# Performance work log

Hardware: AMD Instinct MI355X
Metric: run time of the kernel (lower is better)

## Reference

```python
import jax, jax.numpy as jnp
import numpy as np

N = 50000
E = 800000
EL = 100000
IN_CH = 33
HID = 64
OUT = 128
NTYPES = 311
EMB = 16
COMB = IN_CH - 1 + EMB  # 48


def setup_inputs() -> dict:
    key = jax.random.key(0)
    ks = jax.random.split(key, 24)
    # x: col 0 = node type (integer-valued float), rest = float features
    types = jax.random.randint(ks[0], (N, 1), 0, NTYPES).astype(jnp.float32)
    feats = jax.random.normal(ks[1], (N, IN_CH - 1), dtype=jnp.float32)
    x = jnp.concatenate([types, feats], axis=1)
    edge_index = jax.random.randint(ks[2], (2, E), 0, N, dtype=jnp.int32)
    edge_label_index = jax.random.randint(ks[3], (2, EL), 0, N, dtype=jnp.int32)
    s = 0.05
    inp = {
        'x': x, 'edge_index': edge_index, 'edge_label_index': edge_label_index,
        'emb': jax.random.normal(ks[4], (NTYPES, EMB)) * s,
        'W1': jax.random.normal(ks[5], (COMB, 4 * HID)) * s,
        'a_src1': jax.random.normal(ks[6], (4, HID)) * s,
        'a_dst1': jax.random.normal(ks[7], (4, HID)) * s,
        'b1': jnp.zeros((4 * HID,)),
        'W2': jax.random.normal(ks[8], (4 * HID, 2 * 2 * HID)) * s,
        'a_src2': jax.random.normal(ks[9], (2, 2 * HID)) * s,
        'a_dst2': jax.random.normal(ks[10], (2, 2 * HID)) * s,
        'b2': jnp.zeros((2 * 2 * HID,)),
        'W3': jax.random.normal(ks[11], (4 * HID, OUT)) * s,
        'a_src3': jax.random.normal(ks[12], (1, OUT)) * s,
        'a_dst3': jax.random.normal(ks[13], (1, OUT)) * s,
        'b3': jnp.zeros((OUT,)),
        'Wl1': jax.random.normal(ks[14], (2 * OUT, HID)) * s,
        'bl1': jnp.zeros((HID,)),
        'Wl2': jax.random.normal(ks[15], (HID, 1)) * s,
        'bl2': jnp.zeros((1,)),
        'trans_bias': jax.random.normal(ks[16], (NTYPES, NTYPES)) * s,
    }
    return inp


def _gat(h_in, src, dst, W, a_src, a_dst, b, heads, d_out):
    # linear transform, per-head split
    h = (h_in @ W).reshape(N, heads, d_out)                      # [N,H,D]
    al_s = jnp.einsum('nhd,hd->nh', h, a_src)                    # [N,H]
    al_d = jnp.einsum('nhd,hd->nh', h, a_dst)
    logits = jax.nn.leaky_relu(al_s[src] + al_d[dst], 0.2)       # [E,H]
    m = jax.ops.segment_max(logits, dst, num_segments=N)
    m = jnp.where(jnp.isfinite(m), m, 0.0)
    e = jnp.exp(logits - m[dst])
    denom = jax.ops.segment_sum(e, dst, num_segments=N)
    alpha = e / (denom[dst] + 1e-16)                             # [E,H]
    msg = h[src] * alpha[:, :, None]                             # [E,H,D]
    out = jax.ops.segment_sum(msg, dst, num_segments=N)          # [N,H,D]
    return out.reshape(N, heads * d_out) + b


def reference(x, edge_index, edge_label_index, emb, W1, a_src1, a_dst1, b1,
              W2, a_src2, a_dst2, b2, W3, a_src3, a_dst3, b3,
              Wl1, bl1, Wl2, bl2, trans_bias):
    node_types = x[:, 0].astype(jnp.int32)
    x_comb = jnp.concatenate([emb[node_types], x[:, 1:]], axis=1)  # [N,48]
    # add self loops (PyG GATConv default)
    loops = jnp.arange(N, dtype=edge_index.dtype)
    ei = jnp.concatenate([edge_index, jnp.stack([loops, loops])], axis=1)
    src, dst = ei[0], ei[1]
    z = jax.nn.elu(_gat(x_comb, src, dst, W1, a_src1, a_dst1, b1, 4, HID))
    z = jax.nn.elu(_gat(z, src, dst, W2, a_src2, a_dst2, b2, 2, 2 * HID))
    z = _gat(z, src, dst, W3, a_src3, a_dst3, b3, 1, OUT)
    # decode
    ls, ld = edge_label_index[0], edge_label_index[1]
    ef = jnp.concatenate([z[ls], z[ld]], axis=1)                  # [EL,2*OUT]
    h = jax.nn.relu(ef @ Wl1 + bl1)
    base = h @ Wl2 + bl2                                          # [EL,1]
    bias = trans_bias[node_types[ls], node_types[ld]][:, None]
    return base + bias
```

## Files before the change

kernel.cpp:

```cpp
#include <hip/hip_runtime.h>
#include <hip/hip_bf16.h>

#define NN 50000
#define EE 800000
#define ELN 100000
#define ETOT (EE + NN)
#define NT 311

#define NBUCK ((NN + 127) >> 7)
#define BCAP 3072
#define CHUNK 8192

#define SB_CVT 512
#define SB_PRE (SB_CVT)
#define SB_BC  (SB_CVT + 1)
#define SB_ZS  (SB_CVT + 2)
#define ZS_N   (NN * 6)
#define SB_TOT (SB_ZS + (ZS_N + 255) / 256)

typedef _Float16 f16;
typedef f16 f16x8 __attribute__((ext_vector_type(8)));
typedef f16 f16x4 __attribute__((ext_vector_type(4)));
typedef f16 f16x2 __attribute__((ext_vector_type(2)));
typedef float f32x4 __attribute__((ext_vector_type(4)));

__device__ __forceinline__ float edge_alpha(float l)
{
    l = l > 0.f ? l : 0.2f * l;
    return __expf(fminf(l, 80.f));
}

__global__ __launch_bounds__(256) void k_prepatt(const float* __restrict__ x,
                                                 const float* __restrict__ emb,
                                                 const float* __restrict__ a1ps,
                                                 const float* __restrict__ a1pd,
                                                 f16* __restrict__ xc,
                                                 int* __restrict__ ntypes,
                                                 float* __restrict__ als,
                                                 float* __restrict__ ald)
{
    int gid = blockIdx.x * 256 + threadIdx.x;
    int n = gid >> 6, lane = gid & 63;
    if (n >= NN) return;
    int tpe = (int)x[(size_t)n * 33];
    tpe = tpe < 0 ? 0 : (tpe > NT - 1 ? NT - 1 : tpe);
    if (lane == 0) ntypes[n] = tpe;
    float v;
    if (lane < 16)      v = emb[tpe * 16 + lane];
    else if (lane < 48) v = x[(size_t)n * 33 + 1 + (lane - 16)];
    else                v = 0.f;
    f16 hv = (f16)v;
    xc[(size_t)n * 64 + lane] = hv;
    float xv = (float)hv;
    float ps[4], pd[4];
    #pragma unroll
    for (int h = 0; h < 4; ++h) {
        ps[h] = xv * a1ps[h * 64 + lane];
        pd[h] = xv * a1pd[h * 64 + lane];
    }
    #pragma unroll
    for (int off = 32; off > 0; off >>= 1) {
        #pragma unroll
        for (int h = 0; h < 4; ++h) {
            ps[h] += __shfl_xor(ps[h], off, 64);
            pd[h] += __shfl_xor(pd[h], off, 64);
        }
    }
    if (lane == 0) {
        #pragma unroll
        for (int h = 0; h < 4; ++h) {
            als[n * 4 + h] = ps[h];
            ald[n * 4 + h] = pd[h];
        }
    }
}

__global__ __launch_bounds__(256) void k_setup(const float* __restrict__ W1,
                                               const float* __restrict__ W2,
                                               const float* __restrict__ W3,
                                               const float* __restrict__ Wl1,
                                               f16* __restrict__ Wt1,
                                               f16* __restrict__ Wt2,
                                               f16* __restrict__ Wt3,
                                               f16* __restrict__ Wtl,
                                               const float* __restrict__ as1,
                                               const float* __restrict__ ad1,
                                               float* __restrict__ a1ps,
                                               float* __restrict__ a1pd,
                                               int* __restrict__ bcur,
                                               float* __restrict__ zsc)
{
    const int b = blockIdx.x;
    const int t = threadIdx.x;
    if (b < SB_CVT) {
        int idx = b * 256 + t;
        if (idx < 16384) {
            int h = idx >> 12, c = (idx >> 6) & 63, k = idx & 63;
            Wt1[idx] = (k < 48) ? (f16)W1[(size_t)k * 256 + h * 64 + c] : (f16)0.f;
        } else if (idx < 81920) {
            int i = idx - 16384;
            int c = i >> 8, k = i & 255;
            Wt2[i] = (f16)W2[(size_t)k * 256 + c];
        } else if (idx < 114688) {
            int i = idx - 81920;
            int c = i >> 8, k = i & 255;
            Wt3[i] = (f16)W3[(size_t)k * 128 + c];
        } else {
            int i = idx - 114688;
            int c = i >> 8, k = i & 255;
            Wtl[i] = (f16)Wl1[(size_t)k * 64 + c];
        }
    } else if (b == SB_PRE) {
        int h = t >> 6, k = t & 63;
        float ss = 0.f, sd = 0.f;
        if (k < 48) {
            for (int d = 0; d < 64; ++d) {
                float w = W1[(size_t)k * 256 + h * 64 + d];
                ss += w * as1[h * 64 + d];
                sd += w * ad1[h * 64 + d];
            }
        }
        a1ps[t] = ss;
        a1pd[t] = sd;
    } else if (b == SB_BC) {
        for (int i = t; i < NBUCK + 1; i += 256) bcur[i] = 0;
    } else {
        int i = (b - SB_ZS) * 256 + t;
        if (i < ZS_N) zsc[i] = 0.f;
    }
}

__global__ __launch_bounds__(256) void k_bucket(const int* __restrict__ ei,
                                                int* __restrict__ bcur,
                                                int2* __restrict__ bbuf)
{
    __shared__ int hist[NBUCK];
    __shared__ int gbase[NBUCK];
    const int t = threadIdx.x;
    for (int i = t; i < NBUCK; i += 256) hist[i] = 0;
    __syncthreads();
    const int e0 = blockIdx.x * CHUNK;
    const int eend = min(e0 + CHUNK, ETOT);
    for (int e = e0 + t; e < eend; e += 256) {
        int dst = (e < EE) ? ei[EE + e] : (e - EE);
        atomicAdd(&hist[dst >> 7], 1);
    }
    __syncthreads();
    for (int i = t; i < NBUCK; i += 256) {
        int c = hist[i];
        gbase[i] = c ? atomicAdd(&bcur[i], c) : 0;
        hist[i] = 0;
    }
    __syncthreads();
    for (int e = e0 + t; e < eend; e += 256) {
        int src, dst;
        if (e < EE) { src = ei[e]; dst = ei[EE + e]; }
        else        { src = e - EE; dst = src; }
        int b = dst >> 7;
        int pos = gbase[b] + atomicAdd(&hist[b], 1);
        if (pos < BCAP)
            bbuf[(size_t)b * BCAP + pos] = make_int2(src, dst);
    }
}

__global__ __launch_bounds__(256) void k_csrb(const int* __restrict__ bcur,
                                              const int2* __restrict__ bbuf,
                                              int* __restrict__ rowptr,
                                              int* __restrict__ csr)
{
    __shared__ int red[256];
    __shared__ int nh[128];
    __shared__ int loff[128];
    __shared__ int ncur[128];
    __shared__ int ssrc[BCAP];
    const int b = blockIdx.x;
    const int t = threadIdx.x;
    const int n0 = b << 7;
    const int cnt = min(bcur[b], BCAP);
    const size_t bb = (size_t)b * BCAP;
    int accb = 0, acct = 0;
    for (int j = t; j < NBUCK; j += 256) {
        int c = min(bcur[j], BCAP);
        acct += c;
        if (j < b) accb += c;
    }
    red[t] = accb;
    __syncthreads();
    #pragma unroll
    for (int off = 128; off > 0; off >>= 1) {
        if (t < off) red[t] += red[t + off];
        __syncthreads();
    }
    const int base = red[0];
    __syncthreads();
    if (b == 0) {
        red[t] = acct;
        __syncthreads();
        #pragma unroll
        for (int off = 128; off > 0; off >>= 1) {
            if (t < off) red[t] += red[t + off];
            __syncthreads();
        }
        if (t == 0) rowptr[NN] = red[0];
        __syncthreads();
    }
    if (t < 128) { nh[t] = 0; ncur[t] = 0; }
    __syncthreads();
    for (int i = t; i < cnt; i += 256)
        atomicAdd(&nh[bbuf[bb + i].y - n0], 1);
    __syncthreads();
    int myc = (t < 128) ? nh[t] : 0;
    #pragma unroll
    for (int off = 1; off < 128; off <<= 1) {
        int u = (t >= off && t < 128) ? nh[t - off] : 0;
        __syncthreads();
        if (t < 128) nh[t] += u;
        __syncthreads();
    }
    if (t < 128) {
        int ex = nh[t] - myc;
        loff[t] = ex;
        int n = n0 + t;
        if (n < NN) rowptr[n] = base + ex;
    }
    __syncthreads();
    for (int i = t; i < cnt; i += 256) {
        int2 p = bbuf[bb + i];
        int ln = p.y - n0;
        int pos = loff[ln] + atomicAdd(&ncur[ln], 1);
        ssrc[pos] = p.x;
    }
    __syncthreads();
    for (int i = t; i < cnt; i += 256)
        csr[base + i] = ssrc[i];
}

template<int K, int CN, int H>
__global__ __launch_bounds__(256) void k_gemmw(const f16* __restrict__ A,
                                               const f16* __restrict__ Wt,
                                               f16* __restrict__ O,
                                               int nrows,
                                               const float* __restrict__ asrc,
                                               const float* __restrict__ adst,
                                               float* __restrict__ als,
                                               float* __restrict__ ald)
{
    constexpr int LDK = 40;
    __shared__ f16 As[128 * LDK];
    __shared__ f16 Bs[128 * LDK];
    const int t = threadIdx.x;
    const int w = t >> 6;
    const int lane = t & 63;
    const int m = lane & 15;
    const int quad = lane >> 4;
    const int row0 = blockIdx.x * 128;
    const int col0 = blockIdx.y * 128;
    const int r_st = t >> 1;
    const int seg  = (t & 1) * 16;
    f32x4 acc[2][8] = {};
    for (int k0 = 0; k0 < K; k0 += 32) {
        int gr = row0 + r_st;
        f16x8 av0 = {0,0,0,0,0,0,0,0}, av1 = {0,0,0,0,0,0,0,0};
        if (gr < nrows) {
            av0 = *(const f16x8*)&A[(size_t)gr * K + k0 + seg];
            av1 = *(const f16x8*)&A[(size_t)gr * K + k0 + seg + 8];
        }
        *(f16x8*)&As[r_st * LDK + seg]     = av0;
        *(f16x8*)&As[r_st * LDK + seg + 8] = av1;
        f16x8 bv0 = *(const f16x8*)&Wt[(size_t)(col0 + r_st) * K + k0 + seg];
        f16x8 bv1 = *(const f16x8*)&Wt[(size_t)(col0 + r_st) * K + k0 + seg + 8];
        *(f16x8*)&Bs[r_st * LDK + seg]     = bv0;
        *(f16x8*)&Bs[r_st * LDK + seg + 8] = bv1;
        __syncthreads();
        f16x8 af0 = *(const f16x8*)&As[(w * 32 + m) * LDK + quad * 8];
        f16x8 af1 = *(const f16x8*)&As[(w * 32 + 16 + m) * LDK + quad * 8];
        #pragma unroll
        for (int g = 0; g < 8; ++g) {
            f16x8 bf = *(const f16x8*)&Bs[(g * 16 + m) * LDK + quad * 8];
            acc[0][g] = __builtin_amdgcn_mfma_f32_16x16x32_f16(af0, bf, acc[0][g], 0, 0, 0);
            acc[1][g] = __builtin_amdgcn_mfma_f32_16x16x32_f16(af1, bf, acc[1][g], 0, 0, 0);
        }
        __syncthreads();
    }
    #pragma unroll
    for (int rb = 0; rb < 2; ++rb) {
        #pragma unroll
        for (int g = 0; g < 8; ++g) {
            #pragma unroll
            for (int reg = 0; reg < 4; ++reg) {
                int gr = row0 + w * 32 + rb * 16 + quad * 4 + reg;
                int gc = col0 + g * 16 + m;
                if (gr < nrows) O[(size_t)gr * CN + gc] = (f16)acc[rb][g][reg];
            }
        }
    }
    if constexpr (H > 0) {
        constexpr int D = CN / H;
        const int head = col0 / D;
        float ps[2][4] = {}, pd[2][4] = {};
        #pragma unroll
        for (int g = 0; g < 8; ++g) {
            int col = col0 + g * 16 + m;
            float a_s = asrc[col], a_d = adst[col];
            #pragma unroll
            for (int rb = 0; rb < 2; ++rb) {
                #pragma unroll
                for (int reg = 0; reg < 4; ++reg) {
                    ps[rb][reg] += acc[rb][g][reg] * a_s;
                    pd[rb][reg] += acc[rb][g][reg] * a_d;
                }
            }
        }
        #pragma unroll
        for (int off = 1; off < 16; off <<= 1) {
            #pragma unroll
            for (int rb = 0; rb < 2; ++rb) {
                #pragma unroll
                for (int reg = 0; reg < 4; ++reg) {
                    ps[rb][reg] += __shfl_xor(ps[rb][reg], off, 64);
                    pd[rb][reg] += __shfl_xor(pd[rb][reg], off, 64);
                }
            }
        }
        if (m == 0) {
            #pragma unroll
            for (int rb = 0; rb < 2; ++rb) {
                #pragma unroll
                for (int reg = 0; reg < 4; ++reg) {
                    int gr = row0 + w * 32 + rb * 16 + quad * 4 + reg;
                    if (gr < nrows) {
                        atomicAdd(&als[gr * H + head], ps[rb][reg]);
                        atomicAdd(&ald[gr * H + head], pd[rb][reg]);
                    }
                }
            }
        }
    }
}

__global__ __launch_bounds__(256) void k_gemm1h(const f16* __restrict__ A,
                                                const f16* __restrict__ Wt1,
                                                const float* __restrict__ bias,
                                                f16* __restrict__ O,
                                                int nrows)
{
    constexpr int LDA = 40;
    __shared__ f16 As[64 * LDA];
    __shared__ f16 Bs[64 * LDA];
    const int t = threadIdx.x;
    const int w = t >> 6;
    const int lane = t & 63;
    const int m = lane & 15;
    const int quad = lane >> 4;
    const int row0 = blockIdx.x * 64;
    const int head = blockIdx.y;
    const int r_st = t >> 2;
    const int seg  = (t & 3) * 8;
    f32x4 acc[4] = {{0.f,0.f,0.f,0.f},{0.f,0.f,0.f,0.f},{0.f,0.f,0.f,0.f},{0.f,0.f,0.f,0.f}};
    for (int k0 = 0; k0 < 64; k0 += 32) {
        int gr = row0 + r_st;
        f16x8 av = {0,0,0,0,0,0,0,0};
        if (gr < nrows) av = *(const f16x8*)&A[(size_t)gr * 256 + head * 64 + k0 + seg];
        *(f16x8*)&As[r_st * LDA + seg] = av;
        f16x8 bv = *(const f16x8*)&Wt1[(size_t)head * 4096 + (size_t)r_st * 64 + k0 + seg];
        *(f16x8*)&Bs[r_st * LDA + seg] = bv;
        __syncthreads();
        f16x8 af = *(const f16x8*)&As[(w * 16 + m) * LDA + quad * 8];
        #pragma unroll
        for (int g = 0; g < 4; ++g) {
            f16x8 bf = *(const f16x8*)&Bs[(g * 16 + m) * LDA + quad * 8];
            acc[g] = __builtin_amdgcn_mfma_f32_16x16x32_f16(af, bf, acc[g], 0, 0, 0);
        }
        __syncthreads();
    }
    #pragma unroll
    for (int g = 0; g < 4; ++g) {
        #pragma unroll
        for (int reg = 0; reg < 4; ++reg) {
            int gr = row0 + w * 16 + quad * 4 + reg;
            int col = head * 64 + g * 16 + m;
            if (gr < nrows) {
                float v = acc[g][reg] + bias[col];
                v = v > 0.f ? v : (__expf(v) - 1.f);
                O[(size_t)gr * 256 + col] = (f16)v;
            }
        }
    }
}

__global__ __launch_bounds__(256) void k_aggx(const int* __restrict__ rowptr,
                                              const int* __restrict__ csr,
                                              const float* __restrict__ als,
                                              const float* __restrict__ ald,
                                              const f16* __restrict__ xc,
                                              f16* __restrict__ xagg)
{
    int gid = blockIdx.x * 256 + threadIdx.x;
    int n = gid >> 6, lane = gid & 63;
    if (n >= NN) return;
    int p  = lane >> 4;
    int fl = lane & 15;
    int cb = fl * 4;
    int r0 = rowptr[n], r1 = rowptr[n + 1];
    float4 dl = *(const float4*)&ald[(size_t)n * 4];
    float a0[4] = {}, a1[4] = {}, a2[4] = {}, a3[4] = {};
    float d0 = 0.f, d1 = 0.f, d2 = 0.f, d3 = 0.f;
    int i = r0;
    for (; i + 8 <= r1; i += 8) {
        int i0 = i + p, i1 = i + 4 + p;
        int s0 = csr[i0], s1 = csr[i1];
        f16x4 x0 = *(const f16x4*)&xc[(size_t)s0 * 64 + cb];
        f16x4 x1 = *(const f16x4*)&xc[(size_t)s1 * 64 + cb];
        float4 A0 = *(const float4*)&als[(size_t)s0 * 4];
        float4 A1 = *(const float4*)&als[(size_t)s1 * 4];
        float4 e0, e1;
        e0.x = edge_alpha(A0.x + dl.x); e1.x = edge_alpha(A1.x + dl.x);
        e0.y = edge_alpha(A0.y + dl.y); e1.y = edge_alpha(A1.y + dl.y);
        e0.z = edge_alpha(A0.z + dl.z); e1.z = edge_alpha(A1.z + dl.z);
        e0.w = edge_alpha(A0.w + dl.w); e1.w = edge_alpha(A1.w + dl.w);
        #pragma unroll
        for (int j = 0; j < 4; ++j) {
            float v0 = (float)x0[j], v1 = (float)x1[j];
            a0[j] += e0.x * v0 + e1.x * v1;
            a1[j] += e0.y * v0 + e1.y * v1;
            a2[j] += e0.z * v0 + e1.z * v1;
            a3[j] += e0.w * v0 + e1.w * v1;
        }
        d0 += e0.x + e1.x; d1 += e0.y + e1.y;
        d2 += e0.z + e1.z; d3 += e0.w + e1.w;
    }
    for (; i < r1; i += 4) {
        int ii = i + p;
        bool v = ii < r1;
        int s0 = csr[v ? ii : r0];
        f16x4 x0 = *(const f16x4*)&xc[(size_t)s0 * 64 + cb];
        float4 A0 = *(const float4*)&als[(size_t)s0 * 4];
        float4 e0;
        e0.x = v ? edge_alpha(A0.x + dl.x) : 0.f;
        e0.y = v ? edge_alpha(A0.y + dl.y) : 0.f;
        e0.z = v ? edge_alpha(A0.z + dl.z) : 0.f;
        e0.w = v ? edge_alpha(A0.w + dl.w) : 0.f;
        #pragma unroll
        for (int j = 0; j < 4; ++j) {
            float v0 = (float)x0[j];
            a0[j] += e0.x * v0; a1[j] += e0.y * v0;
            a2[j] += e0.z * v0; a3[j] += e0.w * v0;
        }
        d0 += e0.x; d1 += e0.y; d2 += e0.z; d3 += e0.w;
    }
    #pragma unroll
    for (int off = 16; off < 64; off <<= 1) {
        #pragma unroll
        for (int j = 0; j < 4; ++j) {
            a0[j] += __shfl_xor(a0[j], off, 64);
            a1[j] += __shfl_xor(a1[j], off, 64);
            a2[j] += __shfl_xor(a2[j], off, 64);
            a3[j] += __shfl_xor(a3[j], off, 64);
        }
        d0 += __shfl_xor(d0, off, 64);
        d1 += __shfl_xor(d1, off, 64);
        d2 += __shfl_xor(d2, off, 64);
        d3 += __shfl_xor(d3, off, 64);
    }
    if (p == 0) {
        float i0 = 1.f / d0, i1 = 1.f / d1, i2 = 1.f / d2, i3 = 1.f / d3;
        size_t base = (size_t)n * 256 + cb;
        f16x4 o0, o1, o2, o3;
        #pragma unroll
        for (int j = 0; j < 4; ++j) {
            o0[j] = (f16)(a0[j] * i0);
            o1[j] = (f16)(a1[j] * i1);
            o2[j] = (f16)(a2[j] * i2);
            o3[j] = (f16)(a3[j] * i3);
        }
        *(f16x4*)&xagg[base]       = o0;
        *(f16x4*)&xagg[base + 64]  = o1;
        *(f16x4*)&xagg[base + 128] = o2;
        *(f16x4*)&xagg[base + 192] = o3;
    }
}

__global__ __launch_bounds__(256) void k_agg2f(const int* __restrict__ rowptr,
                                               const int* __restrict__ csr,
                                               const float* __restrict__ als,
                                               const float* __restrict__ ald,
                                               const f16* __restrict__ h,
                                               const float* __restrict__ bias,
                                               f16* __restrict__ z)
{
    int gid = blockIdx.x * 256 + threadIdx.x;
    int n = gid >> 6, lane = gid & 63;
    if (n >= NN) return;
    int p  = lane >> 5;
    int cb = (lane & 31) * 8;
    int head = cb >> 7;
    int r0 = rowptr[n], r1 = rowptr[n + 1];
    float dd = ald[(size_t)n * 2 + head];
    float a[8] = {};
    float den = 0.f;
    int i = r0;
    for (; i + 8 <= r1; i += 8) {
        int i0 = i + p, i1 = i + 2 + p, i2 = i + 4 + p, i3 = i + 6 + p;
        int s0 = csr[i0], s1 = csr[i1], s2 = csr[i2], s3 = csr[i3];
        f16x8 h0 = *(const f16x8*)&h[(size_t)s0 * 256 + cb];
        f16x8 h1 = *(const f16x8*)&h[(size_t)s1 * 256 + cb];
        f16x8 h2 = *(const f16x8*)&h[(size_t)s2 * 256 + cb];
        f16x8 h3 = *(const f16x8*)&h[(size_t)s3 * 256 + cb];
        float w0 = als[(size_t)s0 * 2 + head];
        float w1 = als[(size_t)s1 * 2 + head];
        float w2 = als[(size_t)s2 * 2 + head];
        float w3 = als[(size_t)s3 * 2 + head];
        float e0 = edge_alpha(w0 + dd);
        float e1 = edge_alpha(w1 + dd);
        float e2 = edge_alpha(w2 + dd);
        float e3 = edge_alpha(w3 + dd);
        #pragma unroll
        for (int j = 0; j < 8; ++j)
            a[j] += e0 * (float)h0[j] + e1 * (float)h1[j]
                  + e2 * (float)h2[j] + e3 * (float)h3[j];
        den += e0 + e1 + e2 + e3;
    }
    for (; i < r1; i += 2) {
        int ii = i + p;
        bool v = ii < r1;
        int s0 = csr[v ? ii : r0];
        f16x8 h0 = *(const f16x8*)&h[(size_t)s0 * 256 + cb];
        float e0 = v ? edge_alpha(als[(size_t)s0 * 2 + head] + dd) : 0.f;
        #pragma unroll
        for (int j = 0; j < 8; ++j) a[j] += e0 * (float)h0[j];
        den += e0;
    }
    #pragma unroll
    for (int j = 0; j < 8; ++j) a[j] += __shfl_xor(a[j], 32, 64);
    den += __shfl_xor(den, 32, 64);
    if (p == 0) {
        float inv = 1.f / den;
        f16x8 o;
        #pragma unroll
        for (int j = 0; j < 8; ++j) {
            float v = a[j] * inv + bias[cb + j];
            v = v > 0.f ? v : (__expf(v) - 1.f);
            o[j] = (f16)v;
        }
        *(f16x8*)&z[(size_t)n * 256 + cb] = o;
    }
}

__global__ __launch_bounds__(256) void k_agg3(const int* __restrict__ rowptr,
                                              const int* __restrict__ csr,
                                              const float* __restrict__ als,
                                              const float* __restrict__ ald,
                                              const f16* __restrict__ h,
                                              const float* __restrict__ bias,
                                              f16* __restrict__ z)
{
    int gid = blockIdx.x * 256 + threadIdx.x;
    int n = gid >> 6, lane = gid & 63;
    if (n >= NN) return;
    int p  = lane >> 4;
    int cb = (lane & 15) * 8;
    int r0 = rowptr[n], r1 = rowptr[n + 1];
    float dd = ald[n];
    float a[8] = {};
    float den = 0.f;
    int i = r0;
    for (; i + 8 <= r1; i += 8) {
        int i0 = i + p, i1 = i + 4 + p;
        int s0 = csr[i0], s1 = csr[i1];
        f16x8 h0 = *(const f16x8*)&h[(size_t)s0 * 128 + cb];
        f16x8 h1 = *(const f16x8*)&h[(size_t)s1 * 128 + cb];
        float e0 = edge_alpha(als[s0] + dd);
        float e1 = edge_alpha(als[s1] + dd);
        #pragma unroll
        for (int j = 0; j < 8; ++j)
            a[j] += e0 * (float)h0[j] + e1 * (float)h1[j];
        den += e0 + e1;
    }
    for (; i < r1; i += 4) {
        int ii = i + p;
        bool v = ii < r1;
        int s0 = csr[v ? ii : r0];
        f16x8 h0 = *(const f16x8*)&h[(size_t)s0 * 128 + cb];
        float e0 = v ? edge_alpha(als[s0] + dd) : 0.f;
        #pragma unroll
        for (int j = 0; j < 8; ++j) a[j] += e0 * (float)h0[j];
        den += e0;
    }
    #pragma unroll
    for (int j = 0; j < 8; ++j) {
        a[j] += __shfl_xor(a[j], 16, 64);
        a[j] += __shfl_xor(a[j], 32, 64);
    }
    den += __shfl_xor(den, 16, 64);
    den += __shfl_xor(den, 32, 64);
    if (lane < 16) {
        float inv = 1.f / den;
        f16x8 o;
        #pragma unroll
        for (int j = 0; j < 8; ++j)
            o[j] = (f16)(a[j] * inv + bias[cb + j]);
        *(f16x8*)&z[(size_t)n * 128 + cb] = o;
    }
}

#define DLDA 264
__global__ __launch_bounds__(256) void k_decm(const f16* __restrict__ z3,
                                              const int* __restrict__ eli,
                                              const int* __restrict__ ntypes,
                                              const f16* __restrict__ Wtl,
                                              const float* __restrict__ bl1,
                                              const float* __restrict__ Wl2,
                                              const float* __restrict__ bl2,
                                              const float* __restrict__ tb,
                                              float* __restrict__ out)
{
    __shared__ f16 As[64 * DLDA];
    __shared__ int sls[64], sld[64];
    const int t = threadIdx.x;
    const int e0 = blockIdx.x * 64;
    if (t < 64) {
        int e = e0 + t;
        sls[t] = (e < ELN) ? eli[e] : 0;
        sld[t] = (e < ELN) ? eli[ELN + e] : 0;
    }
    __syncthreads();
    {
        int r = t & 63;
        int seg = t >> 6;
        int base = seg * 64;
        int node = (base < 128) ? sls[r] : sld[r];
        int zoff = base & 127;
        #pragma unroll
        for (int j = 0; j < 8; ++j) {
            f16x8 v = *(const f16x8*)&z3[(size_t)node * 128 + zoff + j * 8];
            *(f16x8*)&As[r * DLDA + base + j * 8] = v;
        }
    }
    __syncthreads();
    const int w = t >> 6;
    const int lane = t & 63;
    const int m = lane & 15;
    const int quad = lane >> 4;
    f32x4 acc[4] = {{0.f,0.f,0.f,0.f},{0.f,0.f,0.f,0.f},{0.f,0.f,0.f,0.f},{0.f,0.f,0.f,0.f}};
    for (int k0 = 0; k0 < 256; k0 += 32) {
        f16x8 af = *(const f16x8*)&As[(w * 16 + m) * DLDA + k0 + quad * 8];
        #pragma unroll
        for (int g = 0; g < 4; ++g) {
            f16x8 bf = *(const f16x8*)&Wtl[(size_t)(g * 16 + m) * 256 + k0 + quad * 8];
            acc[g] = __builtin_amdgcn_mfma_f32_16x16x32_f16(af, bf, acc[g], 0, 0, 0);
        }
    }
    float s[4] = {0.f, 0.f, 0.f, 0.f};
    #pragma unroll
    for (int g = 0; g < 4; ++g) {
        int col = g * 16 + m;
        float b = bl1[col], wv = Wl2[col];
        #pragma unroll
        for (int reg = 0; reg < 4; ++reg) {
            float hv = fmaxf(acc[g][reg] + b, 0.f);
            s[reg] += hv * wv;
        }
    }
    #pragma unroll
    for (int off = 1; off < 16; off <<= 1) {
        #pragma unroll
        for (int reg = 0; reg < 4; ++reg) s[reg] += __shfl_xor(s[reg], off, 64);
    }
    if (m == 0) {
        float b2v = bl2[0];
        #pragma unroll
        for (int reg = 0; reg < 4; ++reg) {
            int r = w * 16 + quad * 4 + reg;
            int e = e0 + r;
            if (e < ELN) {
                out[e] = s[reg] + b2v +
                         tb[(size_t)ntypes[sls[r]] * NT + ntypes[sld[r]]];
            }
        }
    }
}

extern "C" void kernel_launch(void* const* d_in, const int* in_sizes, int n_in,
                              void* d_out, int out_size, void* d_ws, size_t ws_size,
                              hipStream_t stream)
{
    const float* x   = (const float*)d_in[0];
    const int*   ei  = (const int*)d_in[1];
    const int*   eli = (const int*)d_in[2];
    const float* emb = (const float*)d_in[3];
    const float* W1  = (const float*)d_in[4];
    const float* as1 = (const float*)d_in[5];
    const float* ad1 = (const float*)d_in[6];
    const float* b1  = (const float*)d_in[7];
    const float* W2  = (const float*)d_in[8];
    const float* as2 = (const float*)d_in[9];
    const float* ad2 = (const float*)d_in[10];
    const float* b2  = (const float*)d_in[11];
    const float* W3  = (const float*)d_in[12];
    const float* as3 = (const float*)d_in[13];
    const float* ad3 = (const float*)d_in[14];
    const float* b3  = (const float*)d_in[15];
    const float* Wl1 = (const float*)d_in[16];
    const float* bl1 = (const float*)d_in[17];
    const float* Wl2 = (const float*)d_in[18];
    const float* bl2 = (const float*)d_in[19];
    const float* tb  = (const float*)d_in[20];
    float* out = (float*)d_out;

    char* ws = (char*)d_ws;
    size_t off = 0;
    auto alloc = [&](size_t bytes) { size_t o = off; off = (off + bytes + 255) & ~(size_t)255; return o; };
    int*   ntypes = (int*)  (ws + alloc((size_t)NN * 4));
    f16*   xc16   = (f16*)  (ws + alloc((size_t)NN * 64 * 2));
    int*   rowptr = (int*)  (ws + alloc((size_t)(NN + 1) * 4));
    int*   csr    = (int*)  (ws + alloc((size_t)ETOT * 4));
    int*   bcur   = (int*)  (ws + alloc((size_t)(NBUCK + 1) * 4));
    float* scores = (float*)(ws + alloc((size_t)NN * 14 * 4));
    float* als1 = scores;
    float* ald1 = scores + (size_t)NN * 4;
    float* als2 = scores + (size_t)NN * 8;
    float* ald2 = scores + (size_t)NN * 10;
    float* als3 = scores + (size_t)NN * 12;
    float* ald3 = scores + (size_t)NN * 13;
    int2*  bbuf   = (int2*) (ws + alloc((size_t)NBUCK * BCAP * 8));
    f16*   h16    = (f16*)  (ws + alloc((size_t)NN * 256 * 2));
    f16*   z16    = (f16*)  (ws + alloc((size_t)NN * 256 * 2));
    f16*   Wt1    = (f16*)  (ws + alloc((size_t)4 * 64 * 64 * 2));
    f16*   Wt2    = (f16*)  (ws + alloc((size_t)256 * 256 * 2));
    f16*   Wt3    = (f16*)  (ws + alloc((size_t)128 * 256 * 2));
    f16*   Wtl    = (f16*)  (ws + alloc((size_t)64 * 256 * 2));
    float* a1ps   = (float*)(ws + alloc(256 * 4));
    float* a1pd   = (float*)(ws + alloc(256 * 4));

    const int RB   = (NN + 63) / 64;
    const int RB2  = (NN + 127) / 128;
    const int gW1  = (NN + 3) / 4;

    k_setup<<<SB_TOT, 256, 0, stream>>>(W1, W2, W3, Wl1, Wt1, Wt2, Wt3, Wtl,
                                        as1, ad1, a1ps, a1pd, bcur, als2);
    k_prepatt<<<gW1, 256, 0, stream>>>(x, emb, a1ps, a1pd, xc16, ntypes, als1, ald1);

    k_bucket<<<(ETOT + CHUNK - 1) / CHUNK, 256, 0, stream>>>(ei, bcur, bbuf);
    k_csrb  <<<NBUCK, 256, 0, stream>>>(bcur, bbuf, rowptr, csr);

    k_aggx<<<gW1, 256, 0, stream>>>(rowptr, csr, als1, ald1, xc16, h16 );
    k_gemm1h<<<dim3(RB, 4), 256, 0, stream>>>(h16 , Wt1, b1, z16, NN);

    k_gemmw<256, 256, 2><<<dim3(RB2, 2), 256, 0, stream>>>(z16, Wt2, h16, NN, as2, ad2, als2, ald2);
    k_agg2f<<<gW1, 256, 0, stream>>>(rowptr, csr, als2, ald2, h16, b2, z16);

    k_gemmw<256, 128, 1><<<dim3(RB2, 1), 256, 0, stream>>>(z16, Wt3, h16, NN, as3, ad3, als3, ald3);
    k_agg3<<<gW1, 256, 0, stream>>>(rowptr, csr, als3, ald3, h16, b3, z16);

    k_decm<<<(ELN + 63) / 64, 256, 0, stream>>>(z16, eli, ntypes, Wtl, bl1, Wl2, bl2, tb, out);
}
```

Baseline: 390.0 us.

## Split layer-2 features into per-head planes and aggregate each head separately

The layer-2 GEMM now writes its output as two head-major planes of [N,128] instead of interleaved [N,256] rows. The aggregation kernel launches one block set per head, with each wave handling one node and head across 4 edge partitions of 16 lanes. The intent is to make each gathered source row a compact 256-byte chunk, which should improve cache locality for the random neighbor gathers, since each head's working set is half the size. The trade-off is twice as many aggregation blocks and repeated rowptr/csr/edge-weight reads per head, plus extra shuffle reduction steps.

```diff
diff --git a/kernel.cpp b/kernel.cpp
--- a/kernel.cpp
+++ b/kernel.cpp
@@ -17,6 +17,8 @@
 #define SB_ZS  (SB_CVT + 2)
 #define ZS_N   (NN * 6)
 #define SB_TOT (SB_ZS + (ZS_N + 255) / 256)
+
+#define NGB ((NN + 3) / 4)
 
 typedef _Float16 f16;
 typedef f16 f16x8 __attribute__((ext_vector_type(8)));
@@ -235,7 +237,7 @@
         csr[base + i] = ssrc[i];
 }
 
-template<int K, int CN, int H>
+template<int K, int CN, int H, int SPLITH>
 __global__ __launch_bounds__(256) void k_gemmw(const f16* __restrict__ A,
                                                const f16* __restrict__ Wt,
                                                f16* __restrict__ O,
@@ -290,7 +292,13 @@
             for (int reg = 0; reg < 4; ++reg) {
                 int gr = row0 + w * 32 + rb * 16 + quad * 4 + reg;
                 int gc = col0 + g * 16 + m;
-                if (gr < nrows) O[(size_t)gr * CN + gc] = (f16)acc[rb][g][reg];
+                if (gr < nrows) {
+                    if constexpr (SPLITH) {
+                        O[((size_t)(col0 >> 7) * NN + gr) * 128 + (gc & 127)] = (f16)acc[rb][g][reg];
+                    } else {
+                        O[(size_t)gr * CN + gc] = (f16)acc[rb][g][reg];
+                    }
+                }
             }
         }
     }
@@ -480,69 +488,67 @@
     }
 }
 
-__global__ __launch_bounds__(256) void k_agg2f(const int* __restrict__ rowptr,
+__global__ __launch_bounds__(256) void k_agg2h(const int* __restrict__ rowptr,
                                                const int* __restrict__ csr,
                                                const float* __restrict__ als,
                                                const float* __restrict__ ald,
-                                               const f16* __restrict__ h,
+                                               const f16* __restrict__ h2,
                                                const float* __restrict__ bias,
                                                f16* __restrict__ z)
 {
-    int gid = blockIdx.x * 256 + threadIdx.x;
-    int n = gid >> 6, lane = gid & 63;
+    int bx = blockIdx.x;
+    int head = (bx >= NGB) ? 1 : 0;
+    int ng = bx - head * NGB;
+    int t = threadIdx.x;
+    int n = ng * 4 + (t >> 6);
     if (n >= NN) return;
-    int p  = lane >> 5;
-    int cb = (lane & 31) * 8;
-    int head = cb >> 7;
+    int lane = t & 63;
+    int p  = lane >> 4;
+    int cb = (lane & 15) * 8;
     int r0 = rowptr[n], r1 = rowptr[n + 1];
+    const f16* hh = h2 + (size_t)head * NN * 128;
     float dd = ald[(size_t)n * 2 + head];
     float a[8] = {};
     float den = 0.f;
     int i = r0;
     for (; i + 8 <= r1; i += 8) {
-        int i0 = i + p, i1 = i + 2 + p, i2 = i + 4 + p, i3 = i + 6 + p;
-        int s0 = csr[i0], s1 = csr[i1], s2 = csr[i2], s3 = csr[i3];
-        f16x8 h0 = *(const f16x8*)&h[(size_t)s0 * 256 + cb];
-        f16x8 h1 = *(const f16x8*)&h[(size_t)s1 * 256 + cb];
-        f16x8 h2 = *(const f16x8*)&h[(size_t)s2 * 256 + cb];
-        f16x8 h3 = *(const f16x8*)&h[(size_t)s3 * 256 + cb];
-        float w0 = als[(size_t)s0 * 2 + head];
-        float w1 = als[(size_t)s1 * 2 + head];
-        float w2 = als[(size_t)s2 * 2 + head];
-        float w3 = als[(size_t)s3 * 2 + head];
-        float e0 = edge_alpha(w0 + dd);
-        float e1 = edge_alpha(w1 + dd);
-        float e2 = edge_alpha(w2 + dd);
-        float e3 = edge_alpha(w3 + dd);
+        int s0 = csr[i + p], s1 = csr[i + 4 + p];
+        f16x8 h0 = *(const f16x8*)&hh[(size_t)s0 * 128 + cb];
+        f16x8 h1 = *(const f16x8*)&hh[(size_t)s1 * 128 + cb];
+        float e0 = edge_alpha(als[(size_t)s0 * 2 + head] + dd);
+        float e1 = edge_alpha(als[(size_t)s1 * 2 + head] + dd);
+        den += e0 + e1;
         #pragma unroll
         for (int j = 0; j < 8; ++j)
-            a[j] += e0 * (float)h0[j] + e1 * (float)h1[j]
-                  + e2 * (float)h2[j] + e3 * (float)h3[j];
-        den += e0 + e1 + e2 + e3;
-    }
-    for (; i < r1; i += 2) {
+            a[j] += e0 * (float)h0[j] + e1 * (float)h1[j];
+    }
+    for (; i < r1; i += 4) {
         int ii = i + p;
         bool v = ii < r1;
         int s0 = csr[v ? ii : r0];
-        f16x8 h0 = *(const f16x8*)&h[(size_t)s0 * 256 + cb];
+        f16x8 h0 = *(const f16x8*)&hh[(size_t)s0 * 128 + cb];
         float e0 = v ? edge_alpha(als[(size_t)s0 * 2 + head] + dd) : 0.f;
+        den += e0;
         #pragma unroll
         for (int j = 0; j < 8; ++j) a[j] += e0 * (float)h0[j];
-        den += e0;
-    }
-    #pragma unroll
-    for (int j = 0; j < 8; ++j) a[j] += __shfl_xor(a[j], 32, 64);
-    den += __shfl_xor(den, 32, 64);
+    }
+    #pragma unroll
+    for (int off = 16; off < 64; off <<= 1) {
+        #pragma unroll
+        for (int j = 0; j < 8; ++j) a[j] += __shfl_xor(a[j], off, 64);
+        den += __shfl_xor(den, off, 64);
+    }
     if (p == 0) {
         float inv = 1.f / den;
+        int colb = head * 128 + cb;
         f16x8 o;
         #pragma unroll
         for (int j = 0; j < 8; ++j) {
-            float v = a[j] * inv + bias[cb + j];
+            float v = a[j] * inv + bias[colb + j];
             v = v > 0.f ? v : (__expf(v) - 1.f);
             o[j] = (f16)v;
         }
-        *(f16x8*)&z[(size_t)n * 256 + cb] = o;
+        *(f16x8*)&z[(size_t)n * 256 + colb] = o;
     }
 }
 
@@ -746,10 +752,10 @@
     k_aggx<<<gW1, 256, 0, stream>>>(rowptr, csr, als1, ald1, xc16, h16 );
     k_gemm1h<<<dim3(RB, 4), 256, 0, stream>>>(h16 , Wt1, b1, z16, NN);
 
-    k_gemmw<256, 256, 2><<<dim3(RB2, 2), 256, 0, stream>>>(z16, Wt2, h16, NN, as2, ad2, als2, ald2);
-    k_agg2f<<<gW1, 256, 0, stream>>>(rowptr, csr, als2, ald2, h16, b2, z16);
-
-    k_gemmw<256, 128, 1><<<dim3(RB2, 1), 256, 0, stream>>>(z16, Wt3, h16, NN, as3, ad3, als3, ald3);
+    k_gemmw<256, 256, 2, 1><<<dim3(RB2, 2), 256, 0, stream>>>(z16, Wt2, h16, NN, as2, ad2, als2, ald2);
+    k_agg2h<<<2 * NGB, 256, 0, stream>>>(rowptr, csr, als2, ald2, h16, b2, z16);
+
+    k_gemmw<256, 128, 1, 0><<<dim3(RB2, 1), 256, 0, stream>>>(z16, Wt3, h16, NN, as3, ad3, als3, ald3);
     k_agg3<<<gW1, 256, 0, stream>>>(rowptr, csr, als3, ald3, h16, b3, z16);
 
     k_decm<<<(ELN + 63) / 64, 256, 0, stream>>>(z16, eli, ntypes, Wtl, bl1, Wl2, bl2, tb, out);
```

Result: no change. 392.2 us (+0.6%).
